# Kernel optimization log

Measured on AMD Instinct MI355X. Metric: run time of the kernel, lower is better.

## Reference

```python
import jax, jax.numpy as jnp
import numpy as np

LN_EPS = 1e-5


def _layernorm(x, w, b):
    mu = jnp.mean(x, axis=-1, keepdims=True)
    var = jnp.mean((x - mu) ** 2, axis=-1, keepdims=True)
    return (x - mu) * jax.lax.rsqrt(var + LN_EPS) * w + b


def setup_inputs() -> dict:
    key = jax.random.key(0)
    n, d = 512, 256
    ks = jax.random.split(key, 12)
    s = 1.0 / np.sqrt(d)
    inp = {
        "h": jax.random.normal(ks[0], (n, d), dtype=jnp.float32),
        "e": jax.random.normal(ks[1], (n, n, d), dtype=jnp.float32),
        "t_emb": jax.random.normal(ks[2], (d,), dtype=jnp.float32),
        "W1": jax.random.uniform(ks[3], (d, d), jnp.float32, -s, s),
        "W2": jax.random.uniform(ks[4], (d, d), jnp.float32, -s, s),
        "W3": jax.random.uniform(ks[5], (d, d), jnp.float32, -s, s),
        "W_t": jax.random.uniform(ks[6], (d, d), jnp.float32, -s, s),
        "W4": jax.random.uniform(ks[7], (d, d), jnp.float32, -s, s),
        "W5": jax.random.uniform(ks[8], (d, d), jnp.float32, -s, s),
        "gate_w": jax.random.uniform(ks[9], (d, 1), jnp.float32, -s, s),
        "gate_b": jax.random.uniform(ks[10], (1,), jnp.float32, -s, s),
        "ln_e_w": jnp.ones((d,), jnp.float32),
        "ln_e_b": jnp.zeros((d,), jnp.float32),
        "ln_h_w": jnp.ones((d,), jnp.float32),
        "ln_h_b": jnp.zeros((d,), jnp.float32),
    }
    return inp


def reference(h, e, t_emb, W1, W2, W3, W_t, W4, W5, gate_w, gate_b,
              ln_e_w, ln_e_b, ln_h_w, ln_h_b):
    # nn.Linear applies x @ W.T (no bias except gate)
    t_bias = t_emb @ W_t.T                      # (d,)
    hi = (h @ W1.T)[:, None, :]                 # (n,1,d)
    hj = (h @ W2.T)[None, :, :]                 # (1,n,d)
    pre = hi + hj + jnp.einsum('ijd,kd->ijk', e, W3) + t_bias  # (n,n,d)
    e_new = jax.nn.relu(_layernorm(pre, ln_e_w, ln_e_b))       # (n,n,d)
    logits = e_new @ gate_w + gate_b            # (n,n,1)
    eta = jax.nn.softmax(logits, axis=1)        # softmax over j (dim=1)
    agg = jnp.einsum('ijk,ijd,kd->ik', eta * 1.0, e_new, W5) if False else \
          jnp.sum(eta * jnp.einsum('ijd,kd->ijk', e_new, W5), axis=1)  # (n,d)
    h_new = h + jax.nn.relu(_layernorm(h @ W4.T + agg, ln_h_w, ln_h_b))
    return (h_new, e_new)
```

## Files before the change

kernel.cpp:

```cpp
#include <hip/hip_runtime.h>

#define NN 512
#define DD 256

typedef float f32x4 __attribute__((ext_vector_type(4)));
typedef short s16x8 __attribute__((ext_vector_type(8)));

__device__ __forceinline__ unsigned short f2bf(float f) {
    unsigned u = __float_as_uint(f);
    u += 0x7fffu + ((u >> 16) & 1u);
    return (unsigned short)(u >> 16);
}
__device__ __forceinline__ float bf2f(unsigned short s) {
    return __uint_as_float(((unsigned)s) << 16);
}
__device__ __forceinline__ unsigned packbf(float a, float b) {
    return ((unsigned)f2bf(b) << 16) | f2bf(a);
}
__device__ __forceinline__ s16x8 pack_bf(const f32x4 v0, const f32x4 v1) {
    s16x8 a;
    a[0] = (short)f2bf(v0[0]); a[1] = (short)f2bf(v0[1]);
    a[2] = (short)f2bf(v0[2]); a[3] = (short)f2bf(v0[3]);
    a[4] = (short)f2bf(v1[0]); a[5] = (short)f2bf(v1[1]);
    a[6] = (short)f2bf(v1[2]); a[7] = (short)f2bf(v1[3]);
    return a;
}
__device__ __forceinline__ void gl_lds16(const float* g, float* lds) {
    __builtin_amdgcn_global_load_lds(
        (const __attribute__((address_space(1))) void*)g,
        (__attribute__((address_space(3))) void*)lds, 16, 0, 0);
}

__global__ __launch_bounds__(256) void k1_pre(
    const float* __restrict__ h,  const float* __restrict__ W1,
    const float* __restrict__ W2, const float* __restrict__ W4,
    const float* __restrict__ t_emb, const float* __restrict__ W_t,
    const float* __restrict__ W3,
    float* __restrict__ hb, float* __restrict__ hW2, float* __restrict__ hW4,
    unsigned short* __restrict__ w3b,
    float* __restrict__ wacc, float* __restrict__ zacc)
{
    __shared__ float xs[8][DD];
    __shared__ float st[DD];
    const int b = blockIdx.x;
    const int t = threadIdx.x;
    if (b < 64) {
        #pragma unroll
        for (int r = 0; r < 8; ++r) xs[r][t] = h[(size_t)(b * 8 + r) * DD + t];
        st[t] = t_emb[t];
        __syncthreads();
        float a1[8], a2[8], a4[8];
        #pragma unroll
        for (int r = 0; r < 8; ++r) { a1[r] = 0.f; a2[r] = 0.f; a4[r] = 0.f; }
        float tb = 0.f;
        for (int d = 0; d < DD; ++d) {
            const float w1 = W1[(size_t)t * DD + d];
            const float w2 = W2[(size_t)t * DD + d];
            const float w4 = W4[(size_t)t * DD + d];
            tb = fmaf(st[d], W_t[(size_t)t * DD + d], tb);
            #pragma unroll
            for (int r = 0; r < 8; ++r) {
                const float x = xs[r][d];
                a1[r] = fmaf(x, w1, a1[r]);
                a2[r] = fmaf(x, w2, a2[r]);
                a4[r] = fmaf(x, w4, a4[r]);
            }
        }
        #pragma unroll
        for (int r = 0; r < 8; ++r) {
            const size_t o = (size_t)(b * 8 + r) * DD + t;
            hb[o] = a1[r] + tb; hW2[o] = a2[r]; hW4[o] = a4[r];
        }
    } else if (b == 64) {
        for (int c = t; c < DD * DD / 4; c += 256) {
            const f32x4 v = *reinterpret_cast<const f32x4*>(W3 + (size_t)c * 4);
            *reinterpret_cast<uint2*>(w3b + (size_t)c * 4) =
                make_uint2(packbf(v[0], v[1]), packbf(v[2], v[3]));
        }
    } else {
        const f32x4 zero = (f32x4){0.f, 0.f, 0.f, 0.f};
        for (int c = t; c < NN * DD / 4; c += 256)
            *reinterpret_cast<f32x4*>(wacc + (size_t)c * 4) = zero;
        if (t < 256) { zacc[t] = 0.f; zacc[t + 256] = 0.f; }
    }
}

__global__ __launch_bounds__(256) void k2_big(
    const float* __restrict__ e,
    const unsigned short* __restrict__ w3b,
    const float* __restrict__ hb, const float* __restrict__ hW2,
    const float* __restrict__ gate_w, const float* __restrict__ gate_b,
    const float* __restrict__ ln_e_w, const float* __restrict__ ln_e_b,
    float* __restrict__ out_e,
    float* __restrict__ wacc, float* __restrict__ zacc)
{
    const int b = blockIdx.x;
    const int row_base = b * 32;
    const int i = row_base >> 9;
    const int tid = threadIdx.x;
    const int w = tid >> 6;
    const int l = tid & 63;
    const int l15 = l & 15;
    const int lg = l >> 4;

    __shared__ __align__(16) float sAf[32 * 256];
    __shared__ unsigned short s_hbu[DD];
    __shared__ float s_lnw[DD], s_lnb[DD], s_gw[DD];
    __shared__ float s_part[32][4][2];
    __shared__ float s_glog[32][4];

    {
        const float* esrc = e + (size_t)row_base * DD;
        #pragma unroll
        for (int t = 0; t < 8; ++t) {
            const int r = w * 8 + t;
            gl_lds16(esrc + (size_t)r * DD + ((l ^ (r & 7)) << 2), sAf + r * 256);
        }
    }

    const unsigned short* bp = w3b + (size_t)(w * 64 + l15) * DD + lg * 8;
    s16x8 bb[4][4];
    #pragma unroll
    for (int kk = 0; kk < 4; ++kk)
        #pragma unroll
        for (int n = 0; n < 4; ++n)
            bb[kk][n] = *reinterpret_cast<const s16x8*>(bp + (size_t)n * 16 * DD + kk * 32);

    const float gb = gate_b[0];
    s_lnw[tid] = ln_e_w[tid];
    s_lnb[tid] = ln_e_b[tid];
    s_gw[tid]  = gate_w[tid];
    s_hbu[tid] = f2bf(hb[(size_t)i * DD + tid]);
    __syncthreads();

    f32x4 acc[2][4];
    #pragma unroll
    for (int m = 0; m < 2; ++m)
        #pragma unroll
        for (int n = 0; n < 4; ++n)
            acc[m][n] = (f32x4){0.f, 0.f, 0.f, 0.f};

    #pragma unroll
    for (int kk = 0; kk < 8; ++kk) {
        s16x8 afr[2];
        #pragma unroll
        for (int m = 0; m < 2; ++m) {
            const int r = m * 16 + l15;
            const int c0 = kk * 8 + lg * 2;
            const int s0 = c0 ^ (r & 7);
            const int s1 = (c0 + 1) ^ (r & 7);
            const f32x4 v0 = *reinterpret_cast<const f32x4*>(sAf + r * 256 + s0 * 4);
            const f32x4 v1 = *reinterpret_cast<const f32x4*>(sAf + r * 256 + s1 * 4);
            afr[m] = pack_bf(v0, v1);
        }
        #pragma unroll
        for (int n = 0; n < 4; ++n)
            #pragma unroll
            for (int m = 0; m < 2; ++m)
                acc[m][n] = __builtin_amdgcn_mfma_f32_16x16x32_bf16(afr[m], bb[kk & 3][n], acc[m][n], 0, 0, 0);
        if (kk < 4) {
            #pragma unroll
            for (int n = 0; n < 4; ++n)
                bb[kk & 3][n] = *reinterpret_cast<const s16x8*>(bp + (size_t)n * 16 * DD + (kk + 4) * 32);
        }
    }

    float hbn[4];
    #pragma unroll
    for (int n = 0; n < 4; ++n) hbn[n] = bf2f(s_hbu[w * 64 + n * 16 + l15]);

    #pragma unroll
    for (int m = 0; m < 2; ++m) {
        #pragma unroll
        for (int q = 0; q < 4; ++q) {
            const int r = m * 16 + lg * 4 + q;
            const int j = (row_base + r) & 511;
            const float* h2p = hW2 + (size_t)j * DD + w * 64 + l15;
            float s1 = 0.f, s2 = 0.f;
            #pragma unroll
            for (int n = 0; n < 4; ++n) {
                const float v = acc[m][n][q] + hbn[n] + h2p[n * 16];
                acc[m][n][q] = v;
                s1 += v;
                s2 = fmaf(v, v, s2);
            }
            #pragma unroll
            for (int s = 1; s < 16; s <<= 1) {
                s1 += __shfl_xor(s1, s, 64);
                s2 += __shfl_xor(s2, s, 64);
            }
            if (l15 == 0) { s_part[r][w][0] = s1; s_part[r][w][1] = s2; }
        }
    }
    __syncthreads();

    #pragma unroll
    for (int m = 0; m < 2; ++m) {
        #pragma unroll
        for (int q = 0; q < 4; ++q) {
            const int r = m * 16 + lg * 4 + q;
            float S1 = 0.f, S2 = 0.f;
            #pragma unroll
            for (int ww = 0; ww < 4; ++ww) { S1 += s_part[r][ww][0]; S2 += s_part[r][ww][1]; }
            const float mu = S1 * (1.f / 256.f);
            const float rs = rsqrtf(S2 * (1.f / 256.f) - mu * mu + 1e-5f);
            const size_t rowg = (size_t)(row_base + r);
            float gl = 0.f;
            #pragma unroll
            for (int n = 0; n < 4; ++n) {
                const int c = w * 64 + n * 16 + l15;
                float v = (acc[m][n][q] - mu) * rs * s_lnw[c] + s_lnb[c];
                v = fmaxf(v, 0.f);
                acc[m][n][q] = v;
                out_e[rowg * DD + c] = v;
                gl = fmaf(v, s_gw[c], gl);
            }
            #pragma unroll
            for (int s = 1; s < 16; s <<= 1) gl += __shfl_xor(gl, s, 64);
            if (l15 == 0) s_glog[r][w] = gl;
        }
    }
    __syncthreads();

    float p[4] = {0.f, 0.f, 0.f, 0.f};
    float zl = 0.f;
    #pragma unroll
    for (int m = 0; m < 2; ++m) {
        #pragma unroll
        for (int q = 0; q < 4; ++q) {
            const int r = m * 16 + lg * 4 + q;
            const float lv = gb + s_glog[r][0] + s_glog[r][1] + s_glog[r][2] + s_glog[r][3];
            const float ex = __expf(lv);
            zl += ex;
            #pragma unroll
            for (int n = 0; n < 4; ++n) p[n] = fmaf(ex, acc[m][n][q], p[n]);
        }
    }
    #pragma unroll
    for (int n = 0; n < 4; ++n) {
        p[n] += __shfl_xor(p[n], 16, 64);
        p[n] += __shfl_xor(p[n], 32, 64);
    }
    zl += __shfl_xor(zl, 16, 64);
    zl += __shfl_xor(zl, 32, 64);
    if (lg == 0) {
        #pragma unroll
        for (int n = 0; n < 4; ++n)
            atomicAdd(&wacc[(size_t)i * DD + w * 64 + n * 16 + l15], p[n]);
    }
    if (w == 0 && l == 0) atomicAdd(&zacc[i], zl);
}

__global__ __launch_bounds__(256) void k4_final(
    const float* __restrict__ wacc, const float* __restrict__ zacc,
    const float* __restrict__ W5,
    const float* __restrict__ hW4, const float* __restrict__ h,
    const float* __restrict__ ln_h_w, const float* __restrict__ ln_h_b,
    float* __restrict__ out_h)
{
    const int i = blockIdx.x;
    const int k = threadIdx.x;
    __shared__ float xs[DD];
    __shared__ float red[256];

    const float zinv = 1.f / zacc[i];
    xs[k] = wacc[(size_t)i * DD + k] * zinv;
    __syncthreads();
    float a = 0.f;
    for (int d = 0; d < DD; ++d) a = fmaf(xs[d], W5[(size_t)k * DD + d], a);
    const float p = hW4[(size_t)i * DD + k] + a;

    red[k] = p;
    __syncthreads();
    for (int s = 128; s > 0; s >>= 1) {
        if (k < s) red[k] += red[k + s];
        __syncthreads();
    }
    const float mu = red[0] * (1.f / 256.f);
    __syncthreads();
    const float d0 = p - mu;
    red[k] = d0 * d0;
    __syncthreads();
    for (int s = 128; s > 0; s >>= 1) {
        if (k < s) red[k] += red[k + s];
        __syncthreads();
    }
    const float rs = rsqrtf(red[0] * (1.f / 256.f) + 1e-5f);
    float v = d0 * rs * ln_h_w[k] + ln_h_b[k];
    v = fmaxf(v, 0.f);
    out_h[(size_t)i * DD + k] = h[(size_t)i * DD + k] + v;
}

extern "C" void kernel_launch(void* const* d_in, const int* in_sizes, int n_in,
                              void* d_out, int out_size, void* d_ws, size_t ws_size,
                              hipStream_t stream)
{
    const float* h      = (const float*)d_in[0];
    const float* e      = (const float*)d_in[1];
    const float* t_emb  = (const float*)d_in[2];
    const float* W1     = (const float*)d_in[3];
    const float* W2     = (const float*)d_in[4];
    const float* W3     = (const float*)d_in[5];
    const float* W_t    = (const float*)d_in[6];
    const float* W4     = (const float*)d_in[7];
    const float* W5     = (const float*)d_in[8];
    const float* gate_w = (const float*)d_in[9];
    const float* gate_b = (const float*)d_in[10];
    const float* ln_e_w = (const float*)d_in[11];
    const float* ln_e_b = (const float*)d_in[12];
    const float* ln_h_w = (const float*)d_in[13];
    const float* ln_h_b = (const float*)d_in[14];

    float* out_h = (float*)d_out;
    float* out_e = out_h + NN * DD;

    float* wsf  = (float*)d_ws;
    float* hb   = wsf;
    float* hW2  = hb + NN * DD;
    float* hW4  = hW2 + NN * DD;
    float* wacc = hW4 + NN * DD;
    float* zacc = wacc + NN * DD;
    unsigned short* w3b = (unsigned short*)(zacc + NN);

    k1_pre<<<66, 256, 0, stream>>>(h, W1, W2, W4, t_emb, W_t, W3,
                                   hb, hW2, hW4, w3b, wacc, zacc);
    k2_big<<<8192, 256, 0, stream>>>(e, w3b, hb, hW2, gate_w, gate_b,
                                     ln_e_w, ln_e_b, out_e, wacc, zacc);
    k4_final<<<512, 256, 0, stream>>>(wacc, zacc, W5, hW4, h,
                                      ln_h_w, ln_h_b, out_h);
}
```

Baseline: 282.5 us.

## Process four row tiles per block with double-buffered LDS prefetch of e

```diff
diff --git a/kernel.cpp b/kernel.cpp
--- a/kernel.cpp
+++ b/kernel.cpp
@@ -30,6 +30,12 @@
         (const __attribute__((address_space(1))) void*)g,
         (__attribute__((address_space(3))) void*)lds, 16, 0, 0);
 }
+
+#define LDS_SYNC() do {                                          \
+    asm volatile("s_waitcnt lgkmcnt(0)" ::: "memory");           \
+    __builtin_amdgcn_s_barrier();                                \
+    __builtin_amdgcn_sched_barrier(0);                           \
+} while (0)
 
 __global__ __launch_bounds__(256) void k1_pre(
     const float* __restrict__ h,  const float* __restrict__ W1,
@@ -94,148 +100,173 @@
     float* __restrict__ out_e,
     float* __restrict__ wacc, float* __restrict__ zacc)
 {
-    const int b = blockIdx.x;
-    const int row_base = b * 32;
-    const int i = row_base >> 9;
+    const int blk = blockIdx.x;
+    const int row0 = blk * 128;
+    const int i = row0 >> 9;
     const int tid = threadIdx.x;
     const int w = tid >> 6;
     const int l = tid & 63;
     const int l15 = l & 15;
     const int lg = l >> 4;
 
-    __shared__ __align__(16) float sAf[32 * 256];
+    __shared__ __align__(16) float sAf[2][32 * 256];
     __shared__ unsigned short s_hbu[DD];
     __shared__ float s_lnw[DD], s_lnb[DD], s_gw[DD];
     __shared__ float s_part[32][4][2];
     __shared__ float s_glog[32][4];
 
-    {
-        const float* esrc = e + (size_t)row_base * DD;
-        #pragma unroll
-        for (int t = 0; t < 8; ++t) {
-            const int r = w * 8 + t;
-            gl_lds16(esrc + (size_t)r * DD + ((l ^ (r & 7)) << 2), sAf + r * 256);
-        }
-    }
-
-    const unsigned short* bp = w3b + (size_t)(w * 64 + l15) * DD + lg * 8;
-    s16x8 bb[4][4];
-    #pragma unroll
-    for (int kk = 0; kk < 4; ++kk)
-        #pragma unroll
-        for (int n = 0; n < 4; ++n)
-            bb[kk][n] = *reinterpret_cast<const s16x8*>(bp + (size_t)n * 16 * DD + kk * 32);
-
-    const float gb = gate_b[0];
+    auto issue_dma = [&](int tt, int bufsel) {
+        const float* esrc = e + (size_t)(row0 + tt * 32) * DD;
+        #pragma unroll
+        for (int t8 = 0; t8 < 8; ++t8) {
+            const int r = w * 8 + t8;
+            gl_lds16(esrc + (size_t)r * DD + ((l ^ (r & 7)) << 2),
+                     &sAf[bufsel][r * 256]);
+        }
+    };
+
+    issue_dma(0, 0);
     s_lnw[tid] = ln_e_w[tid];
     s_lnb[tid] = ln_e_b[tid];
     s_gw[tid]  = gate_w[tid];
     s_hbu[tid] = f2bf(hb[(size_t)i * DD + tid]);
-    __syncthreads();
-
-    f32x4 acc[2][4];
-    #pragma unroll
-    for (int m = 0; m < 2; ++m)
-        #pragma unroll
-        for (int n = 0; n < 4; ++n)
-            acc[m][n] = (f32x4){0.f, 0.f, 0.f, 0.f};
-
-    #pragma unroll
-    for (int kk = 0; kk < 8; ++kk) {
-        s16x8 afr[2];
-        #pragma unroll
-        for (int m = 0; m < 2; ++m) {
-            const int r = m * 16 + l15;
-            const int c0 = kk * 8 + lg * 2;
-            const int s0 = c0 ^ (r & 7);
-            const int s1 = (c0 + 1) ^ (r & 7);
-            const f32x4 v0 = *reinterpret_cast<const f32x4*>(sAf + r * 256 + s0 * 4);
-            const f32x4 v1 = *reinterpret_cast<const f32x4*>(sAf + r * 256 + s1 * 4);
-            afr[m] = pack_bf(v0, v1);
-        }
-        #pragma unroll
-        for (int n = 0; n < 4; ++n)
-            #pragma unroll
-            for (int m = 0; m < 2; ++m)
-                acc[m][n] = __builtin_amdgcn_mfma_f32_16x16x32_bf16(afr[m], bb[kk & 3][n], acc[m][n], 0, 0, 0);
-        if (kk < 4) {
-            #pragma unroll
-            for (int n = 0; n < 4; ++n)
-                bb[kk & 3][n] = *reinterpret_cast<const s16x8*>(bp + (size_t)n * 16 * DD + (kk + 4) * 32);
-        }
-    }
-
+    const float gb = gate_b[0];
+    issue_dma(1, 1);
+    asm volatile("s_waitcnt vmcnt(8) lgkmcnt(0)" ::: "memory");
+    __builtin_amdgcn_s_barrier();
+    __builtin_amdgcn_sched_barrier(0);
+
+    const unsigned short* bp = w3b + (size_t)(w * 64 + l15) * DD + lg * 8;
+
+    float p[4] = {0.f, 0.f, 0.f, 0.f};
+    float zl = 0.f;
     float hbn[4];
     #pragma unroll
     for (int n = 0; n < 4; ++n) hbn[n] = bf2f(s_hbu[w * 64 + n * 16 + l15]);
 
     #pragma unroll
-    for (int m = 0; m < 2; ++m) {
-        #pragma unroll
-        for (int q = 0; q < 4; ++q) {
-            const int r = m * 16 + lg * 4 + q;
-            const int j = (row_base + r) & 511;
-            const float* h2p = hW2 + (size_t)j * DD + w * 64 + l15;
-            float s1 = 0.f, s2 = 0.f;
-            #pragma unroll
-            for (int n = 0; n < 4; ++n) {
-                const float v = acc[m][n][q] + hbn[n] + h2p[n * 16];
-                acc[m][n][q] = v;
-                s1 += v;
-                s2 = fmaf(v, v, s2);
-            }
-            #pragma unroll
-            for (int s = 1; s < 16; s <<= 1) {
-                s1 += __shfl_xor(s1, s, 64);
-                s2 += __shfl_xor(s2, s, 64);
-            }
-            if (l15 == 0) { s_part[r][w][0] = s1; s_part[r][w][1] = s2; }
-        }
-    }
-    __syncthreads();
-
-    #pragma unroll
-    for (int m = 0; m < 2; ++m) {
-        #pragma unroll
-        for (int q = 0; q < 4; ++q) {
-            const int r = m * 16 + lg * 4 + q;
-            float S1 = 0.f, S2 = 0.f;
-            #pragma unroll
-            for (int ww = 0; ww < 4; ++ww) { S1 += s_part[r][ww][0]; S2 += s_part[r][ww][1]; }
-            const float mu = S1 * (1.f / 256.f);
-            const float rs = rsqrtf(S2 * (1.f / 256.f) - mu * mu + 1e-5f);
-            const size_t rowg = (size_t)(row_base + r);
-            float gl = 0.f;
-            #pragma unroll
-            for (int n = 0; n < 4; ++n) {
-                const int c = w * 64 + n * 16 + l15;
-                float v = (acc[m][n][q] - mu) * rs * s_lnw[c] + s_lnb[c];
-                v = fmaxf(v, 0.f);
-                acc[m][n][q] = v;
-                out_e[rowg * DD + c] = v;
-                gl = fmaf(v, s_gw[c], gl);
-            }
-            #pragma unroll
-            for (int s = 1; s < 16; s <<= 1) gl += __shfl_xor(gl, s, 64);
-            if (l15 == 0) s_glog[r][w] = gl;
-        }
-    }
-    __syncthreads();
-
-    float p[4] = {0.f, 0.f, 0.f, 0.f};
-    float zl = 0.f;
-    #pragma unroll
-    for (int m = 0; m < 2; ++m) {
-        #pragma unroll
-        for (int q = 0; q < 4; ++q) {
-            const int r = m * 16 + lg * 4 + q;
-            const float lv = gb + s_glog[r][0] + s_glog[r][1] + s_glog[r][2] + s_glog[r][3];
-            const float ex = __expf(lv);
-            zl += ex;
-            #pragma unroll
-            for (int n = 0; n < 4; ++n) p[n] = fmaf(ex, acc[m][n][q], p[n]);
-        }
-    }
+    for (int t = 0; t < 4; ++t) {
+        const int cur = t & 1;
+        const int row_base = row0 + t * 32;
+        const float* sA = sAf[cur];
+
+        s16x8 bb[4][4];
+        #pragma unroll
+        for (int kk = 0; kk < 4; ++kk)
+            #pragma unroll
+            for (int n = 0; n < 4; ++n)
+                bb[kk][n] = *reinterpret_cast<const s16x8*>(bp + (size_t)n * 16 * DD + kk * 32);
+
+        f32x4 acc[2][4];
+        #pragma unroll
+        for (int m = 0; m < 2; ++m)
+            #pragma unroll
+            for (int n = 0; n < 4; ++n)
+                acc[m][n] = (f32x4){0.f, 0.f, 0.f, 0.f};
+
+        #pragma unroll
+        for (int kk = 0; kk < 8; ++kk) {
+            s16x8 afr[2];
+            #pragma unroll
+            for (int m = 0; m < 2; ++m) {
+                const int r = m * 16 + l15;
+                const int c0 = kk * 8 + lg * 2;
+                const int s0 = c0 ^ (r & 7);
+                const int s1 = (c0 + 1) ^ (r & 7);
+                const f32x4 v0 = *reinterpret_cast<const f32x4*>(sA + r * 256 + s0 * 4);
+                const f32x4 v1 = *reinterpret_cast<const f32x4*>(sA + r * 256 + s1 * 4);
+                afr[m] = pack_bf(v0, v1);
+            }
+            #pragma unroll
+            for (int n = 0; n < 4; ++n)
+                #pragma unroll
+                for (int m = 0; m < 2; ++m)
+                    acc[m][n] = __builtin_amdgcn_mfma_f32_16x16x32_bf16(afr[m], bb[kk & 3][n], acc[m][n], 0, 0, 0);
+            if (kk < 4) {
+                #pragma unroll
+                for (int n = 0; n < 4; ++n)
+                    bb[kk & 3][n] = *reinterpret_cast<const s16x8*>(bp + (size_t)n * 16 * DD + (kk + 4) * 32);
+            }
+        }
+
+        #pragma unroll
+        for (int m = 0; m < 2; ++m) {
+            #pragma unroll
+            for (int q = 0; q < 4; ++q) {
+                const int r = m * 16 + lg * 4 + q;
+                const int j = (row_base + r) & 511;
+                const float* h2p = hW2 + (size_t)j * DD + w * 64 + l15;
+                float s1 = 0.f, s2 = 0.f;
+                #pragma unroll
+                for (int n = 0; n < 4; ++n) {
+                    const float v = acc[m][n][q] + hbn[n] + h2p[n * 16];
+                    acc[m][n][q] = v;
+                    s1 += v;
+                    s2 = fmaf(v, v, s2);
+                }
+                #pragma unroll
+                for (int s = 1; s < 16; s <<= 1) {
+                    s1 += __shfl_xor(s1, s, 64);
+                    s2 += __shfl_xor(s2, s, 64);
+                }
+                if (l15 == 0) { s_part[r][w][0] = s1; s_part[r][w][1] = s2; }
+            }
+        }
+        LDS_SYNC();
+
+        #pragma unroll
+        for (int m = 0; m < 2; ++m) {
+            #pragma unroll
+            for (int q = 0; q < 4; ++q) {
+                const int r = m * 16 + lg * 4 + q;
+                float S1 = 0.f, S2 = 0.f;
+                #pragma unroll
+                for (int ww = 0; ww < 4; ++ww) { S1 += s_part[r][ww][0]; S2 += s_part[r][ww][1]; }
+                const float mu = S1 * (1.f / 256.f);
+                const float rs = rsqrtf(S2 * (1.f / 256.f) - mu * mu + 1e-5f);
+                const size_t rowg = (size_t)(row_base + r);
+                float gl = 0.f;
+                #pragma unroll
+                for (int n = 0; n < 4; ++n) {
+                    const int c = w * 64 + n * 16 + l15;
+                    float v = (acc[m][n][q] - mu) * rs * s_lnw[c] + s_lnb[c];
+                    v = fmaxf(v, 0.f);
+                    acc[m][n][q] = v;
+                    out_e[rowg * DD + c] = v;
+                    gl = fmaf(v, s_gw[c], gl);
+                }
+                #pragma unroll
+                for (int s = 1; s < 16; s <<= 1) gl += __shfl_xor(gl, s, 64);
+                if (l15 == 0) s_glog[r][w] = gl;
+            }
+        }
+        LDS_SYNC();
+
+        #pragma unroll
+        for (int m = 0; m < 2; ++m) {
+            #pragma unroll
+            for (int q = 0; q < 4; ++q) {
+                const int r = m * 16 + lg * 4 + q;
+                const float lv = gb + s_glog[r][0] + s_glog[r][1] + s_glog[r][2] + s_glog[r][3];
+                const float ex = __expf(lv);
+                zl += ex;
+                #pragma unroll
+                for (int n = 0; n < 4; ++n) p[n] = fmaf(ex, acc[m][n][q], p[n]);
+            }
+        }
+
+        if (t < 2) issue_dma(t + 2, cur);
+        if (t == 0 || t == 1) {
+            asm volatile("s_waitcnt vmcnt(8) lgkmcnt(0)" ::: "memory");
+            __builtin_amdgcn_s_barrier();
+            __builtin_amdgcn_sched_barrier(0);
+        } else if (t == 2) {
+            asm volatile("s_waitcnt vmcnt(0) lgkmcnt(0)" ::: "memory");
+            __builtin_amdgcn_s_barrier();
+            __builtin_amdgcn_sched_barrier(0);
+        }
+    }
+
     #pragma unroll
     for (int n = 0; n < 4; ++n) {
         p[n] += __shfl_xor(p[n], 16, 64);
@@ -324,7 +355,7 @@
 
     k1_pre<<<66, 256, 0, stream>>>(h, W1, W2, W4, t_emb, W_t, W3,
                                    hb, hW2, hW4, w3b, wacc, zacc);
-    k2_big<<<8192, 256, 0, stream>>>(e, w3b, hb, hW2, gate_w, gate_b,
+    k2_big<<<2048, 256, 0, stream>>>(e, w3b, hb, hW2, gate_w, gate_b,
                                      ln_e_w, ln_e_b, out_e, wacc, zacc);
     k4_final<<<512, 256, 0, stream>>>(wacc, zacc, W5, hW4, h,
                                       ln_h_w, ln_h_b, out_h);
```

New measurement: 408.0 us. +44.4%, slower.

## Split k2 tile into two 16-row halves to overlap second load with compute

Applied to the files above, without the earlier changes.

```diff
diff --git a/kernel.cpp b/kernel.cpp
--- a/kernel.cpp
+++ b/kernel.cpp
@@ -30,6 +30,12 @@
         (const __attribute__((address_space(1))) void*)g,
         (__attribute__((address_space(3))) void*)lds, 16, 0, 0);
 }
+
+#define LDS_SYNC() do {                                          \
+    asm volatile("s_waitcnt lgkmcnt(0)" ::: "memory");           \
+    __builtin_amdgcn_s_barrier();                                \
+    __builtin_amdgcn_sched_barrier(0);                           \
+} while (0)
 
 __global__ __launch_bounds__(256) void k1_pre(
     const float* __restrict__ h,  const float* __restrict__ W1,
@@ -94,93 +100,95 @@
     float* __restrict__ out_e,
     float* __restrict__ wacc, float* __restrict__ zacc)
 {
-    const int b = blockIdx.x;
-    const int row_base = b * 32;
-    const int i = row_base >> 9;
+    const int blk = blockIdx.x;
+    const int row0 = blk * 32;
+    const int i = row0 >> 9;
     const int tid = threadIdx.x;
     const int w = tid >> 6;
     const int l = tid & 63;
     const int l15 = l & 15;
     const int lg = l >> 4;
 
-    __shared__ __align__(16) float sAf[32 * 256];
+    __shared__ __align__(16) float sAf[2][16 * 256];
     __shared__ unsigned short s_hbu[DD];
     __shared__ float s_lnw[DD], s_lnb[DD], s_gw[DD];
-    __shared__ float s_part[32][4][2];
-    __shared__ float s_glog[32][4];
+    __shared__ float s_part[16][4][2];
+    __shared__ float s_glog[16][4];
 
     {
-        const float* esrc = e + (size_t)row_base * DD;
-        #pragma unroll
-        for (int t = 0; t < 8; ++t) {
-            const int r = w * 8 + t;
-            gl_lds16(esrc + (size_t)r * DD + ((l ^ (r & 7)) << 2), sAf + r * 256);
-        }
-    }
-
-    const unsigned short* bp = w3b + (size_t)(w * 64 + l15) * DD + lg * 8;
-    s16x8 bb[4][4];
-    #pragma unroll
-    for (int kk = 0; kk < 4; ++kk)
-        #pragma unroll
-        for (int n = 0; n < 4; ++n)
-            bb[kk][n] = *reinterpret_cast<const s16x8*>(bp + (size_t)n * 16 * DD + kk * 32);
-
-    const float gb = gate_b[0];
+        const float* esrc = e + (size_t)row0 * DD;
+        #pragma unroll
+        for (int t4 = 0; t4 < 4; ++t4) {
+            const int r = w * 4 + t4;
+            gl_lds16(esrc + (size_t)r * DD + ((l ^ (r & 7)) << 2), &sAf[0][r * 256]);
+        }
+        #pragma unroll
+        for (int t4 = 0; t4 < 4; ++t4) {
+            const int r = w * 4 + t4;
+            gl_lds16(esrc + (size_t)(16 + r) * DD + ((l ^ (r & 7)) << 2), &sAf[1][r * 256]);
+        }
+    }
     s_lnw[tid] = ln_e_w[tid];
     s_lnb[tid] = ln_e_b[tid];
     s_gw[tid]  = gate_w[tid];
     s_hbu[tid] = f2bf(hb[(size_t)i * DD + tid]);
-    __syncthreads();
-
-    f32x4 acc[2][4];
-    #pragma unroll
-    for (int m = 0; m < 2; ++m)
-        #pragma unroll
-        for (int n = 0; n < 4; ++n)
-            acc[m][n] = (f32x4){0.f, 0.f, 0.f, 0.f};
-
-    #pragma unroll
-    for (int kk = 0; kk < 8; ++kk) {
-        s16x8 afr[2];
-        #pragma unroll
-        for (int m = 0; m < 2; ++m) {
-            const int r = m * 16 + l15;
-            const int c0 = kk * 8 + lg * 2;
-            const int s0 = c0 ^ (r & 7);
-            const int s1 = (c0 + 1) ^ (r & 7);
-            const f32x4 v0 = *reinterpret_cast<const f32x4*>(sAf + r * 256 + s0 * 4);
-            const f32x4 v1 = *reinterpret_cast<const f32x4*>(sAf + r * 256 + s1 * 4);
-            afr[m] = pack_bf(v0, v1);
-        }
-        #pragma unroll
-        for (int n = 0; n < 4; ++n)
-            #pragma unroll
-            for (int m = 0; m < 2; ++m)
-                acc[m][n] = __builtin_amdgcn_mfma_f32_16x16x32_bf16(afr[m], bb[kk & 3][n], acc[m][n], 0, 0, 0);
-        if (kk < 4) {
-            #pragma unroll
-            for (int n = 0; n < 4; ++n)
-                bb[kk & 3][n] = *reinterpret_cast<const s16x8*>(bp + (size_t)n * 16 * DD + (kk + 4) * 32);
-        }
-    }
-
+    const float gb = gate_b[0];
+    asm volatile("s_waitcnt vmcnt(4) lgkmcnt(0)" ::: "memory");
+    __builtin_amdgcn_s_barrier();
+    __builtin_amdgcn_sched_barrier(0);
+
+    const unsigned short* bp = w3b + (size_t)(w * 64 + l15) * DD + lg * 8;
     float hbn[4];
     #pragma unroll
     for (int n = 0; n < 4; ++n) hbn[n] = bf2f(s_hbu[w * 64 + n * 16 + l15]);
 
-    #pragma unroll
-    for (int m = 0; m < 2; ++m) {
+    float p[4] = {0.f, 0.f, 0.f, 0.f};
+    float zl = 0.f;
+
+    for (int t = 0; t < 2; ++t) {
+        if (t == 1) __syncthreads();
+        const int row_base = row0 + t * 16;
+        const float* sA = sAf[t];
+
+        s16x8 bb[4][4];
+        #pragma unroll
+        for (int kk = 0; kk < 4; ++kk)
+            #pragma unroll
+            for (int n = 0; n < 4; ++n)
+                bb[kk][n] = *reinterpret_cast<const s16x8*>(bp + (size_t)n * 16 * DD + kk * 32);
+
+        f32x4 acc[4];
+        #pragma unroll
+        for (int n = 0; n < 4; ++n) acc[n] = (f32x4){0.f, 0.f, 0.f, 0.f};
+
+        #pragma unroll
+        for (int kk = 0; kk < 8; ++kk) {
+            const int c0 = kk * 8 + lg * 2;
+            const int s0 = c0 ^ (l15 & 7);
+            const int s1 = (c0 + 1) ^ (l15 & 7);
+            const f32x4 v0 = *reinterpret_cast<const f32x4*>(sA + l15 * 256 + s0 * 4);
+            const f32x4 v1 = *reinterpret_cast<const f32x4*>(sA + l15 * 256 + s1 * 4);
+            const s16x8 afr = pack_bf(v0, v1);
+            #pragma unroll
+            for (int n = 0; n < 4; ++n)
+                acc[n] = __builtin_amdgcn_mfma_f32_16x16x32_bf16(afr, bb[kk & 3][n], acc[n], 0, 0, 0);
+            if (kk < 4) {
+                #pragma unroll
+                for (int n = 0; n < 4; ++n)
+                    bb[kk & 3][n] = *reinterpret_cast<const s16x8*>(bp + (size_t)n * 16 * DD + (kk + 4) * 32);
+            }
+        }
+
         #pragma unroll
         for (int q = 0; q < 4; ++q) {
-            const int r = m * 16 + lg * 4 + q;
+            const int r = lg * 4 + q;
             const int j = (row_base + r) & 511;
             const float* h2p = hW2 + (size_t)j * DD + w * 64 + l15;
             float s1 = 0.f, s2 = 0.f;
             #pragma unroll
             for (int n = 0; n < 4; ++n) {
-                const float v = acc[m][n][q] + hbn[n] + h2p[n * 16];
-                acc[m][n][q] = v;
+                const float v = acc[n][q] + hbn[n] + h2p[n * 16];
+                acc[n][q] = v;
                 s1 += v;
                 s2 = fmaf(v, v, s2);
             }
@@ -191,14 +199,11 @@
             }
             if (l15 == 0) { s_part[r][w][0] = s1; s_part[r][w][1] = s2; }
         }
-    }
-    __syncthreads();
-
-    #pragma unroll
-    for (int m = 0; m < 2; ++m) {
+        LDS_SYNC();
+
         #pragma unroll
         for (int q = 0; q < 4; ++q) {
-            const int r = m * 16 + lg * 4 + q;
+            const int r = lg * 4 + q;
             float S1 = 0.f, S2 = 0.f;
             #pragma unroll
             for (int ww = 0; ww < 4; ++ww) { S1 += s_part[r][ww][0]; S2 += s_part[r][ww][1]; }
@@ -209,9 +214,9 @@
             #pragma unroll
             for (int n = 0; n < 4; ++n) {
                 const int c = w * 64 + n * 16 + l15;
-                float v = (acc[m][n][q] - mu) * rs * s_lnw[c] + s_lnb[c];
+                float v = (acc[n][q] - mu) * rs * s_lnw[c] + s_lnb[c];
                 v = fmaxf(v, 0.f);
-                acc[m][n][q] = v;
+                acc[n][q] = v;
                 out_e[rowg * DD + c] = v;
                 gl = fmaf(v, s_gw[c], gl);
             }
@@ -219,23 +224,19 @@
             for (int s = 1; s < 16; s <<= 1) gl += __shfl_xor(gl, s, 64);
             if (l15 == 0) s_glog[r][w] = gl;
         }
-    }
-    __syncthreads();
-
-    float p[4] = {0.f, 0.f, 0.f, 0.f};
-    float zl = 0.f;
-    #pragma unroll
-    for (int m = 0; m < 2; ++m) {
+        LDS_SYNC();
+
         #pragma unroll
         for (int q = 0; q < 4; ++q) {
-            const int r = m * 16 + lg * 4 + q;
+            const int r = lg * 4 + q;
             const float lv = gb + s_glog[r][0] + s_glog[r][1] + s_glog[r][2] + s_glog[r][3];
             const float ex = __expf(lv);
             zl += ex;
             #pragma unroll
-            for (int n = 0; n < 4; ++n) p[n] = fmaf(ex, acc[m][n][q], p[n]);
-        }
-    }
+            for (int n = 0; n < 4; ++n) p[n] = fmaf(ex, acc[n][q], p[n]);
+        }
+    }
+
     #pragma unroll
     for (int n = 0; n < 4; ++n) {
         p[n] += __shfl_xor(p[n], 16, 64);
```

New measurement: 322.0 us. 14.0% more time.
